# Optimization experiments

Measured on AMD Instinct MI355X. Metric: run time of the kernel, lower is better.

## Reference

```python
import jax, jax.numpy as jnp
import numpy as np

T, I, H, O, M = 1024, 128, 512, 512, 32768
BETA = 8.0


def setup_inputs() -> dict:
    key = jax.random.key(0)
    ks = jax.random.split(key, 8)
    s = 0.05  # small init scale to keep tanh unsaturated
    return {
        "inp": jax.random.normal(ks[0], (T, I), jnp.float32),
        "x_obs": jax.nn.softmax(jax.random.normal(ks[1], (T, O), jnp.float32), axis=-1),
        "patterns": jax.random.normal(ks[2], (M, O + H), jnp.float32),  # stored [x | g] slots
        "last_hidden": jnp.zeros((H,), jnp.float32),
        "W_ih": jax.random.normal(ks[3], (H, I), jnp.float32) * s,
        "W_hh": jax.random.normal(ks[4], (H, H), jnp.float32) * s,
        "b_ih": jax.random.normal(ks[5], (H,), jnp.float32) * s,
        "b_hh": jax.random.normal(ks[6], (H,), jnp.float32) * s,
    }


def _retrieve(query, keys, values, beta):
    # distance-based slot attention: softmax(-beta * ||q - k||^2) @ values
    # sqdist via the expanded form to avoid a [T, M, D] intermediate
    d = (jnp.sum(query * query, axis=-1, keepdims=True)
         + jnp.sum(keys * keys, axis=-1)[None, :]
         - 2.0 * query @ keys.T)  # [T, M]
    w = jax.nn.softmax(-beta * d, axis=-1)
    return w @ values  # [T, O]


def reference(inp, x_obs, patterns, last_hidden, W_ih, W_hh, b_ih, b_hh):
    # single-layer tanh RNN (nn.RNN semantics), unbatched [T, I]
    def step(h, x):
        h_new = jnp.tanh(x @ W_ih.T + b_ih + h @ W_hh.T + b_hh)
        return h_new, h_new

    h_last, g_cur = jax.lax.scan(step, last_hidden, inp)  # g_cur: [T, H]

    x_vals = patterns[:, :O]   # stored x-parts
    g_keys = patterns[:, O:]   # stored g-parts
    prob_g = _retrieve(g_cur, g_keys, x_vals, BETA)   # index_g=True
    prob_x = _retrieve(x_obs, x_vals, x_vals, BETA)   # index_g=False
    # memory.store(hstack([x_obs, g_cur])) is a pure side effect on the buffer
    # and does not affect this step's outputs.
    return prob_g, prob_x, g_cur, h_last[None, :]
```

## Files before the change

### kernel.cpp

```cpp
#include <hip/hip_runtime.h>
#include <math.h>

#define T_STEPS 1024
#define I_DIM   128
#define H_DIM   512
#define O_DIM   512
#define M_PAT   32768
#define SCAN_WGS 8
#define VT_STR  32800

typedef __attribute__((ext_vector_type(8))) short s16x8;
typedef __attribute__((ext_vector_type(4))) float f32x4;

__device__ __forceinline__ void bf_split(float f, unsigned short& hi, unsigned short& lo) {
  unsigned u = __builtin_bit_cast(unsigned, f);
  hi = (unsigned short)(u >> 16);
  float r = f - __builtin_bit_cast(float, u & 0xFFFF0000u);
  lo = (unsigned short)(__builtin_bit_cast(unsigned, r) >> 16);
}
__device__ __forceinline__ unsigned short f2bf(float f) {
  return (unsigned short)(__builtin_bit_cast(unsigned, f) >> 16);
}
__device__ __forceinline__ float bf2f(unsigned short b) {
  return __builtin_bit_cast(float, ((unsigned)b) << 16);
}

__global__ __launch_bounds__(256) void xw_kernel(const float* __restrict__ inp,
    const float* __restrict__ W_ih, const float* __restrict__ b_ih,
    const float* __restrict__ b_hh, float* __restrict__ xw) {
  int t = blockIdx.x;
  __shared__ float4 xs4[I_DIM / 4];
  if (threadIdx.x < I_DIM / 4)
    xs4[threadIdx.x] = ((const float4*)(inp + (size_t)t * I_DIM))[threadIdx.x];
  __syncthreads();
  for (int j = threadIdx.x; j < H_DIM; j += 256) {
    const float4* w4 = (const float4*)(W_ih + (size_t)j * I_DIM);
    float acc = 0.f;
#pragma unroll
    for (int i = 0; i < I_DIM / 4; i++) {
      float4 w = w4[i]; float4 x = xs4[i];
      acc += w.x * x.x + w.y * x.y + w.z * x.z + w.w * x.w;
    }
    xw[(size_t)t * H_DIM + j] = acc + b_ih[j] + b_hh[j];
  }
}

__global__ __launch_bounds__(256, 1) void scan_kernel(
    const float* __restrict__ W_hh, const float* __restrict__ xw,
    const float* __restrict__ h0, float* __restrict__ g_cur,
    float* __restrict__ h_last, unsigned* __restrict__ sync,
    unsigned* __restrict__ henc) {
  unsigned* cnt  = sync + 64;
  unsigned* dec  = sync + 128;
  __shared__ int role_s;
  if (threadIdx.x == 0) {
    unsigned xcd = __builtin_amdgcn_s_getreg(6164) & 7u;
    unsigned my_idx = __hip_atomic_fetch_add(&cnt[xcd], 1u, __ATOMIC_ACQ_REL,
                                             __HIP_MEMORY_SCOPE_AGENT);
    if (blockIdx.x == 0) {
      int chosen = -1;
      while (chosen < 0) {
        for (int x = 0; x < 8; x++)
          if (__hip_atomic_load(&cnt[x], __ATOMIC_ACQUIRE,
                                __HIP_MEMORY_SCOPE_AGENT) >= 8u) { chosen = x; break; }
        if (chosen < 0) __builtin_amdgcn_s_sleep(2);
      }
      __hip_atomic_store(dec, 1u + (unsigned)chosen, __ATOMIC_RELEASE,
                         __HIP_MEMORY_SCOPE_AGENT);
    }
    unsigned d;
    while ((d = __hip_atomic_load(dec, __ATOMIC_ACQUIRE,
                                  __HIP_MEMORY_SCOPE_AGENT)) == 0u)
      __builtin_amdgcn_s_sleep(2);
    role_s = (xcd == d - 1u && my_idx < 8u) ? (int)my_idx : -1;
  }
  __syncthreads();
  const int role = role_s;
  if (role < 0) return;

  const int lane = threadIdx.x & 63;
  const int part = threadIdx.x >> 6;
  const int row  = role * 64 + lane;

  float4 w[32];
  const float4* wsrc = (const float4*)(W_hh + (size_t)row * H_DIM + part * 128);
#pragma unroll
  for (int i = 0; i < 32; i++) w[i] = wsrc[i];
#pragma unroll
  for (int i = 0; i < 32; i++) {
    asm volatile("" : "+v"(w[i].x), "+v"(w[i].y), "+v"(w[i].z), "+v"(w[i].w));
  }

  __shared__ float h_sf[H_DIM];
  __shared__ float red[4][64];

  float xw_next = xw[row];

  for (int t = 0; t < T_STEPS; t++) {
    float xwv = xw_next;
    if (part == 0 && t + 1 < T_STEPS)
      xw_next = xw[(size_t)(t + 1) * H_DIM + row];

    if (t == 0) {
      h_sf[threadIdx.x]       = h0[threadIdx.x];
      h_sf[256 + threadIdx.x] = h0[256 + threadIdx.x];
    } else {
      const unsigned* src = henc + (size_t)(t - 1) * H_DIM;
      unsigned v0, v1;
      do {
        v0 = __hip_atomic_load(src + threadIdx.x, __ATOMIC_RELAXED,
                               __HIP_MEMORY_SCOPE_AGENT);
      } while (__builtin_bit_cast(float, v0) < 1.0f);
      do {
        v1 = __hip_atomic_load(src + 256 + threadIdx.x, __ATOMIC_RELAXED,
                               __HIP_MEMORY_SCOPE_AGENT);
      } while (__builtin_bit_cast(float, v1) < 1.0f);
      h_sf[threadIdx.x]       = __builtin_bit_cast(float, v0) - 2.0f;
      h_sf[256 + threadIdx.x] = __builtin_bit_cast(float, v1) - 2.0f;
    }
    __syncthreads();

    const float4* h4 = (const float4*)h_sf + part * 32;
    float a0 = 0.f, a1 = 0.f, a2 = 0.f, a3 = 0.f;
#pragma unroll
    for (int i = 0; i < 8; i++) {
      float4 x0 = h4[4 * i], x1 = h4[4 * i + 1], x2 = h4[4 * i + 2], x3 = h4[4 * i + 3];
      float4 w0 = w[4 * i], w1 = w[4 * i + 1], w2 = w[4 * i + 2], w3 = w[4 * i + 3];
      a0 += x0.x * w0.x + x0.y * w0.y + x0.z * w0.z + x0.w * w0.w;
      a1 += x1.x * w1.x + x1.y * w1.y + x1.z * w1.z + x1.w * w1.w;
      a2 += x2.x * w2.x + x2.y * w2.y + x2.z * w2.z + x2.w * w2.w;
      a3 += x3.x * w3.x + x3.y * w3.y + x3.z * w3.z + x3.w * w3.w;
    }
    red[part][lane] = (a0 + a1) + (a2 + a3);
    __syncthreads();

    if (part == 0) {
      float pre = red[0][lane] + red[1][lane] + red[2][lane] + red[3][lane] + xwv;
      float e = __expf(2.f * pre);
      float h = 1.f - 2.f / (e + 1.f);
      __hip_atomic_store(henc + (size_t)t * H_DIM + row,
                         __builtin_bit_cast(unsigned, h + 2.0f),
                         __ATOMIC_RELAXED, __HIP_MEMORY_SCOPE_AGENT);
      g_cur[(size_t)t * H_DIM + row] = h;
      if (t == T_STEPS - 1) h_last[row] = h;
    }
  }
}

__global__ __launch_bounds__(256) void norms_kernel(const float* __restrict__ patterns,
    float* __restrict__ bkx, float* __restrict__ bkg) {
  int lane = threadIdx.x & 63;
  int m = blockIdx.x * 4 + (threadIdx.x >> 6);
  const float4* row = (const float4*)(patterns + (size_t)m * (O_DIM + H_DIM));
  float ax = 0.f, ag = 0.f;
#pragma unroll
  for (int jj = 0; jj < 4; jj++) {
    float4 v = row[lane + 64 * jj];
    float s = v.x * v.x + v.y * v.y + v.z * v.z + v.w * v.w;
    if (jj < 2) ax += s; else ag += s;
  }
#pragma unroll
  for (int off = 1; off < 64; off <<= 1) {
    ax += __shfl_xor(ax, off, 64);
    ag += __shfl_xor(ag, off, 64);
  }
  if (lane == 0) { bkx[m] = 8.f * ax; bkg[m] = 8.f * ag; }
}

__global__ __launch_bounds__(256) void vt_kernel(const float* __restrict__ patterns,
                                                 unsigned short* __restrict__ Vt) {
  __shared__ unsigned short tile[64 * 68];
  int kt = blockIdx.x;
  int vt = blockIdx.y;
#pragma unroll
  for (int i = 0; i < 4; i++) {
    int f = threadIdx.x + 256 * i;
    int key = f >> 4, c4 = f & 15;
    float4 v = *(const float4*)(patterns + (size_t)(kt * 64 + key) * 1024 + vt * 64 + c4 * 4);
    unsigned short* dst = &tile[key * 68 + c4 * 4];
    dst[0] = f2bf(v.x); dst[1] = f2bf(v.y); dst[2] = f2bf(v.z); dst[3] = f2bf(v.w);
  }
  __syncthreads();
  int vd = threadIdx.x >> 2, q4 = threadIdx.x & 3;
  unsigned short tmp[16];
#pragma unroll
  for (int k = 0; k < 16; k++) tmp[k] = tile[(q4 * 16 + k) * 68 + vd];
  size_t ob = (size_t)(vt * 64 + vd) * VT_STR + kt * 64 + q4 * 16;
#pragma unroll
  for (int h = 0; h < 2; h++) {
    s16x8 pk;
#pragma unroll
    for (int j = 0; j < 8; j++) pk[j] = (short)tmp[h * 8 + j];
    *(s16x8*)&Vt[ob + h * 8] = pk;
  }
}

template <bool USE_VT>
__global__ __launch_bounds__(512, 2) void flash_kernel(
    const float* __restrict__ Qg, const float* __restrict__ Qx,
    const float* __restrict__ patterns, const float* __restrict__ bkx,
    const float* __restrict__ bkg, const unsigned short* __restrict__ Vt,
    float* __restrict__ pacc, float* __restrict__ pml, int S) {
  const int bid  = blockIdx.x;
  const int sidx = bid >> 6;
  const int ret  = (bid >> 5) & 1;
  const int qt   = bid & 31;
  const int qbase = qt * 32;

  const float* Qp  = ret ? Qx : Qg;
  const float* Kp  = patterns + (ret ? 0 : O_DIM);
  const float* bkk = ret ? bkx : bkg;

  const int chunk = M_PAT / S;
  const int kbeg = sidx * chunk, kend = kbeg + chunk;

  const int lane = threadIdx.x & 63;
  const int wid  = threadIdx.x >> 6;
  const int qg   = wid >> 2;
  const int kw   = wid & 3;
  const int quad = lane >> 4;
  const int l16  = lane & 15;

  __shared__ unsigned short stage_u16[16384];
  __shared__ unsigned short p_lds[32 * 72];
  __shared__ float mrow_s[32], lrow_s[32], alpha_s[32];
  __shared__ int flag_s;

  const int qrow = qbase + qg * 16 + l16;
  s16x8 qhi[16], qlo[16];
#pragma unroll
  for (int kst = 0; kst < 16; kst++) {
    const float4* src = (const float4*)(Qp + (size_t)qrow * 512 + kst * 32 + quad * 8);
    float4 a = src[0], b = src[1];
    float fv[8] = {a.x, a.y, a.z, a.w, b.x, b.y, b.z, b.w};
    s16x8 h, l;
#pragma unroll
    for (int j = 0; j < 8; j++) {
      unsigned short hb, lb; bf_split(fv[j], hb, lb);
      h[j] = (short)hb; l[j] = (short)lb;
    }
    qhi[kst] = h; qlo[kst] = l;
  }

  if (threadIdx.x < 32) { mrow_s[threadIdx.x] = -INFINITY; lrow_s[threadIdx.x] = 0.f; }

  f32x4 o[8];
#pragma unroll
  for (int nb = 0; nb < 8; nb++) o[nb] = (f32x4){0.f, 0.f, 0.f, 0.f};
  float ov[32];
  if (!USE_VT) {
#pragma unroll
    for (int j = 0; j < 32; j++) ov[j] = 0.f;
  }
  const int row2 = threadIdx.x >> 4;
  const int c0   = threadIdx.x & 15;

  for (int k0 = kbeg; k0 < kend; k0 += 64) {
    f32x4 sc = (f32x4){0.f, 0.f, 0.f, 0.f};
#pragma unroll
    for (int dc = 0; dc < 4; dc++) {
      __syncthreads();
      if (dc == 0 && threadIdx.x == 0) flag_s = 0;
#pragma unroll
      for (int i = 0; i < 2; i++) {
        int oid = threadIdx.x + 512 * i;
        int key = oid >> 4, oct = oid & 15;
        const float4* src = (const float4*)(Kp + (size_t)(k0 + key) * 1024 + dc * 128 + oct * 8);
        float4 a = src[0], b = src[1];
        float fv[8] = {a.x, a.y, a.z, a.w, b.x, b.y, b.z, b.w};
        s16x8 hv, lv;
#pragma unroll
        for (int j = 0; j < 8; j++) {
          unsigned short hb, lb; bf_split(fv[j], hb, lb);
          hv[j] = (short)hb; lv[j] = (short)lb;
        }
        int base = (key * 16 + (oct ^ (key & 7))) * 8;
        *(s16x8*)&stage_u16[base] = hv;
        *(s16x8*)&stage_u16[8192 + base] = lv;
      }
      __syncthreads();
#pragma unroll
      for (int ks = 0; ks < 4; ks++) {
        int kst = dc * 4 + ks;
        int key = kw * 16 + l16;
        int oct = ks * 4 + quad;
        int base = (key * 16 + (oct ^ (key & 7))) * 8;
        s16x8 kh = *(const s16x8*)&stage_u16[base];
        s16x8 kl = *(const s16x8*)&stage_u16[8192 + base];
        sc = __builtin_amdgcn_mfma_f32_16x16x32_bf16(qhi[kst], kh, sc, 0, 0, 0);
        sc = __builtin_amdgcn_mfma_f32_16x16x32_bf16(qlo[kst], kh, sc, 0, 0, 0);
        sc = __builtin_amdgcn_mfma_f32_16x16x32_bf16(qhi[kst], kl, sc, 0, 0, 0);
      }
    }
    float bkv = bkk[k0 + kw * 16 + l16];
    __syncthreads();
    float* S_f = (float*)stage_u16;
#pragma unroll
    for (int r = 0; r < 4; r++)
      S_f[(qg * 16 + quad * 4 + r) * 68 + kw * 16 + l16] = 16.f * sc[r] - bkv;
    __syncthreads();

    float s4[4], p4[4];
#pragma unroll
    for (int c = 0; c < 4; c++) s4[c] = S_f[row2 * 68 + c0 + 16 * c];
    float tmax = fmaxf(fmaxf(s4[0], s4[1]), fmaxf(s4[2], s4[3]));
#pragma unroll
    for (int off = 1; off < 16; off <<= 1) tmax = fmaxf(tmax, __shfl_xor(tmax, off, 16));
    float mold = mrow_s[row2];
    float mnew = fmaxf(mold, tmax);
    float tsum = 0.f;
#pragma unroll
    for (int c = 0; c < 4; c++) { p4[c] = __expf(s4[c] - mnew); tsum += p4[c]; }
#pragma unroll
    for (int off = 1; off < 16; off <<= 1) tsum += __shfl_xor(tsum, off, 16);
#pragma unroll
    for (int c = 0; c < 4; c++) p_lds[row2 * 72 + c0 + 16 * c] = f2bf(p4[c]);
    if (c0 == 0) {
      float al = __expf(mold - mnew);
      alpha_s[row2] = al;
      mrow_s[row2] = mnew;
      lrow_s[row2] = lrow_s[row2] * al + tsum;
      if (tmax > mold - 25.f) flag_s = 1;
    }
    __syncthreads();
    const int doPV = flag_s;

    if (doPV) {
      if (USE_VT) {
        float alr[4];
#pragma unroll
        for (int r = 0; r < 4; r++) alr[r] = alpha_s[qg * 16 + quad * 4 + r];
#pragma unroll
        for (int nb = 0; nb < 8; nb++) {
          o[nb][0] *= alr[0]; o[nb][1] *= alr[1]; o[nb][2] *= alr[2]; o[nb][3] *= alr[3];
        }
#pragma unroll
        for (int ks2 = 0; ks2 < 2; ks2++) {
          s16x8 pf = *(const s16x8*)&p_lds[(qg * 16 + l16) * 72 + ks2 * 32 + quad * 8];
#pragma unroll
          for (int nb = 0; nb < 8; nb++) {
            int vd = kw * 128 + nb * 16 + l16;
            s16x8 vf = *(const s16x8*)(Vt + (size_t)vd * VT_STR + (k0 + ks2 * 32 + quad * 8));
            o[nb] = __builtin_amdgcn_mfma_f32_16x16x32_bf16(pf, vf, o[nb], 0, 0, 0);
          }
        }
      } else {
        float al = alpha_s[row2];
#pragma unroll
        for (int j = 0; j < 32; j++) ov[j] *= al;
        for (int key = 0; key < 64; key++) {
          float w = bf2f(p_lds[row2 * 72 + key]);
          const float4* vsrc = (const float4*)(patterns + (size_t)(k0 + key) * 1024 + c0 * 32);
#pragma unroll
          for (int j = 0; j < 8; j++) {
            float4 v = vsrc[j];
            ov[4 * j + 0] += w * v.x; ov[4 * j + 1] += w * v.y;
            ov[4 * j + 2] += w * v.z; ov[4 * j + 3] += w * v.w;
          }
        }
      }
    }
  }

  __syncthreads();
  size_t pbase = ((size_t)(ret * S + sidx) * T_STEPS + qbase);
  if (USE_VT) {
#pragma unroll
    for (int nb = 0; nb < 8; nb++)
#pragma unroll
      for (int r = 0; r < 4; r++)
        pacc[(pbase + qg * 16 + quad * 4 + r) * 512 + kw * 128 + nb * 16 + l16] = o[nb][r];
  } else {
#pragma unroll
    for (int j = 0; j < 32; j++)
      pacc[(pbase + row2) * 512 + c0 * 32 + j] = ov[j];
  }
  if (threadIdx.x < 32) {
    pml[(pbase + threadIdx.x) * 2]     = mrow_s[threadIdx.x];
    pml[(pbase + threadIdx.x) * 2 + 1] = lrow_s[threadIdx.x];
  }
}

__global__ __launch_bounds__(256) void combine_kernel(
    const float* __restrict__ pacc, const float* __restrict__ pml,
    float* __restrict__ out, int S) {
  int b = blockIdx.x;
  int ret = b >> 10, r = b & 1023;
  float M = -INFINITY;
  for (int s = 0; s < S; s++)
    M = fmaxf(M, pml[((size_t)(ret * S + s) * T_STEPS + r) * 2]);
  float L = 0.f;
  for (int s = 0; s < S; s++) {
    size_t mb = ((size_t)(ret * S + s) * T_STEPS + r) * 2;
    L += pml[mb + 1] * __expf(pml[mb] - M);
  }
  float inv = 1.0f / L;
  for (int cc = threadIdx.x; cc < 512; cc += 256) {
    float acc = 0.f;
    for (int s = 0; s < S; s++) {
      size_t mb = ((size_t)(ret * S + s) * T_STEPS + r) * 2;
      float sc = __expf(pml[mb] - M);
      acc += sc * pacc[((size_t)(ret * S + s) * T_STEPS + r) * 512 + cc];
    }
    out[(size_t)ret * (T_STEPS * O_DIM) + (size_t)r * 512 + cc] = acc * inv;
  }
}

extern "C" void kernel_launch(void* const* d_in, const int* in_sizes, int n_in,
                              void* d_out, int out_size, void* d_ws, size_t ws_size,
                              hipStream_t stream) {
  const float* inp      = (const float*)d_in[0];
  const float* x_obs    = (const float*)d_in[1];
  const float* patterns = (const float*)d_in[2];
  const float* h0       = (const float*)d_in[3];
  const float* W_ih     = (const float*)d_in[4];
  const float* W_hh     = (const float*)d_in[5];
  const float* b_ih     = (const float*)d_in[6];
  const float* b_hh     = (const float*)d_in[7];

  float* out    = (float*)d_out;
  float* g_cur  = out + 1048576;
  float* h_last = out + 1572864;

  char* wsb = (char*)d_ws;
  size_t off = 0;
  auto alloc = [&](size_t bytes) -> char* {
    char* p = wsb + off; off += (bytes + 255) & ~(size_t)255; return p;
  };
  unsigned* sync = (unsigned*)alloc(8192);
  unsigned* henc = (unsigned*)alloc((size_t)T_STEPS * H_DIM * 4);
  float* xw  = (float*)alloc((size_t)T_STEPS * H_DIM * 4);
  float* bkx = (float*)alloc((size_t)M_PAT * 4);
  float* bkg = (float*)alloc((size_t)M_PAT * 4);
  size_t base = off;

  const size_t vt_bytes = (size_t)512 * VT_STR * 2;
  auto pml_bytes  = [](int S) { return (size_t)2 * S * T_STEPS * 2 * 4; };
  auto pacc_bytes = [](int S) { return (size_t)2 * S * T_STEPS * 512 * 4; };

  int S = 4; bool use_vt = false;
  if (base + pml_bytes(4) + pacc_bytes(4) + vt_bytes + 1024 <= ws_size) { S = 4; use_vt = true; }
  else if (base + pml_bytes(2) + pacc_bytes(2) + vt_bytes + 1024 <= ws_size) { S = 2; use_vt = true; }
  else if (base + pml_bytes(4) + pacc_bytes(4) + 1024 <= ws_size) { S = 4; use_vt = false; }
  else if (base + pml_bytes(2) + pacc_bytes(2) + 1024 <= ws_size) { S = 2; use_vt = false; }
  else { S = 1; use_vt = false; }

  float* pml  = (float*)alloc(pml_bytes(S));
  float* pacc = (float*)alloc(pacc_bytes(S));
  unsigned short* Vt = use_vt ? (unsigned short*)alloc(vt_bytes) : (unsigned short*)nullptr;

  hipMemsetAsync(sync, 0, 8192, stream);
  hipMemsetAsync(henc, 0, (size_t)T_STEPS * H_DIM * 4, stream);
  xw_kernel<<<T_STEPS, 256, 0, stream>>>(inp, W_ih, b_ih, b_hh, xw);
  scan_kernel<<<128, 256, 0, stream>>>(W_hh, xw, h0, g_cur, h_last, sync, henc);
  norms_kernel<<<M_PAT / 4, 256, 0, stream>>>(patterns, bkx, bkg);
  if (use_vt) {
    vt_kernel<<<dim3(512, 8), 256, 0, stream>>>(patterns, Vt);
    flash_kernel<true><<<S * 64, 512, 0, stream>>>(g_cur, x_obs, patterns, bkx, bkg,
                                                   Vt, pacc, pml, S);
  } else {
    flash_kernel<false><<<S * 64, 512, 0, stream>>>(g_cur, x_obs, patterns, bkx, bkg,
                                                    nullptr, pacc, pml, S);
  }
  combine_kernel<<<2 * T_STEPS, 256, 0, stream>>>(pacc, pml, out, S);
}
```

Before: 2.621 ms.

## Split scan into 32 single-wave workgroups and drop block barriers

Restructures the sequential RNN scan from 8 workgroups of 4 waves to 32 single-wave workgroups on one XCD. Each wave handles 16 rows, with 4 lanes per row each holding a 128-column slice of W_hh in registers, and reduces with intra-wave shuffles instead of an LDS reduction and __syncthreads. Each lane polls 8 h values at once and writes them to a padded LDS buffer, so the per-step block barriers are replaced by an lgkmcnt wait. The aim is shorter per-step critical-path latency, at the cost of more workgroups polling global memory and more scattered polling loads per lane.

New measurement: 2.624 ms. No clear change (+0.1%).

```diff
diff --git a/kernel.cpp b/kernel.cpp
--- a/kernel.cpp
+++ b/kernel.cpp
@@ -6,7 +6,7 @@
 #define H_DIM   512
 #define O_DIM   512
 #define M_PAT   32768
-#define SCAN_WGS 8
+#define SCAN_ROLES 32
 #define VT_STR  32800
 
 typedef __attribute__((ext_vector_type(8))) short s16x8;
@@ -45,7 +45,7 @@
   }
 }
 
-__global__ __launch_bounds__(256, 1) void scan_kernel(
+__global__ __launch_bounds__(64, 1) void scan_kernel(
     const float* __restrict__ W_hh, const float* __restrict__ xw,
     const float* __restrict__ h0, float* __restrict__ g_cur,
     float* __restrict__ h_last, unsigned* __restrict__ sync,
@@ -62,7 +62,9 @@
       while (chosen < 0) {
         for (int x = 0; x < 8; x++)
           if (__hip_atomic_load(&cnt[x], __ATOMIC_ACQUIRE,
-                                __HIP_MEMORY_SCOPE_AGENT) >= 8u) { chosen = x; break; }
+                                __HIP_MEMORY_SCOPE_AGENT) >= (unsigned)SCAN_ROLES) {
+            chosen = x; break;
+          }
         if (chosen < 0) __builtin_amdgcn_s_sleep(2);
       }
       __hip_atomic_store(dec, 1u + (unsigned)chosen, __ATOMIC_RELEASE,
@@ -72,18 +74,18 @@
     while ((d = __hip_atomic_load(dec, __ATOMIC_ACQUIRE,
                                   __HIP_MEMORY_SCOPE_AGENT)) == 0u)
       __builtin_amdgcn_s_sleep(2);
-    role_s = (xcd == d - 1u && my_idx < 8u) ? (int)my_idx : -1;
+    role_s = (xcd == d - 1u && my_idx < (unsigned)SCAN_ROLES) ? (int)my_idx : -1;
   }
   __syncthreads();
   const int role = role_s;
   if (role < 0) return;
 
-  const int lane = threadIdx.x & 63;
-  const int part = threadIdx.x >> 6;
-  const int row  = role * 64 + lane;
+  const int lane = threadIdx.x;
+  const int g    = lane & 3;
+  const int row  = role * 16 + (lane >> 2);
 
   float4 w[32];
-  const float4* wsrc = (const float4*)(W_hh + (size_t)row * H_DIM + part * 128);
+  const float4* wsrc = (const float4*)(W_hh + (size_t)row * H_DIM + g * 128);
 #pragma unroll
   for (int i = 0; i < 32; i++) w[i] = wsrc[i];
 #pragma unroll
@@ -91,51 +93,64 @@
     asm volatile("" : "+v"(w[i].x), "+v"(w[i].y), "+v"(w[i].z), "+v"(w[i].w));
   }
 
-  __shared__ float h_sf[H_DIM];
-  __shared__ float red[4][64];
+  __shared__ float hbuf[528];
 
   float xw_next = xw[row];
 
   for (int t = 0; t < T_STEPS; t++) {
     float xwv = xw_next;
-    if (part == 0 && t + 1 < T_STEPS)
+    if (t + 1 < T_STEPS)
       xw_next = xw[(size_t)(t + 1) * H_DIM + row];
 
     if (t == 0) {
-      h_sf[threadIdx.x]       = h0[threadIdx.x];
-      h_sf[256 + threadIdx.x] = h0[256 + threadIdx.x];
+#pragma unroll
+      for (int j = 0; j < 8; j++) {
+        int c = 64 * j + lane;
+        hbuf[c + 4 * (j >> 1)] = h0[c];
+      }
     } else {
       const unsigned* src = henc + (size_t)(t - 1) * H_DIM;
-      unsigned v0, v1;
-      do {
-        v0 = __hip_atomic_load(src + threadIdx.x, __ATOMIC_RELAXED,
-                               __HIP_MEMORY_SCOPE_AGENT);
-      } while (__builtin_bit_cast(float, v0) < 1.0f);
-      do {
-        v1 = __hip_atomic_load(src + 256 + threadIdx.x, __ATOMIC_RELAXED,
-                               __HIP_MEMORY_SCOPE_AGENT);
-      } while (__builtin_bit_cast(float, v1) < 1.0f);
-      h_sf[threadIdx.x]       = __builtin_bit_cast(float, v0) - 2.0f;
-      h_sf[256 + threadIdx.x] = __builtin_bit_cast(float, v1) - 2.0f;
-    }
-    __syncthreads();
-
-    const float4* h4 = (const float4*)h_sf + part * 32;
+      unsigned u[8];
+#pragma unroll
+      for (int j = 0; j < 8; j++)
+        u[j] = __hip_atomic_load(src + 64 * j + lane, __ATOMIC_RELAXED,
+                                 __HIP_MEMORY_SCOPE_AGENT);
+      bool again = true;
+      while (again) {
+        again = false;
+#pragma unroll
+        for (int j = 0; j < 8; j++)
+          if (__builtin_bit_cast(float, u[j]) < 1.0f) {
+            again = true;
+            u[j] = __hip_atomic_load(src + 64 * j + lane, __ATOMIC_RELAXED,
+                                     __HIP_MEMORY_SCOPE_AGENT);
+          }
+      }
+#pragma unroll
+      for (int j = 0; j < 8; j++) {
+        int c = 64 * j + lane;
+        hbuf[c + 4 * (j >> 1)] = __builtin_bit_cast(float, u[j]) - 2.0f;
+      }
+    }
+    asm volatile("s_waitcnt lgkmcnt(0)" ::: "memory");
+
+    const float4* hb = (const float4*)&hbuf[g * 132];
     float a0 = 0.f, a1 = 0.f, a2 = 0.f, a3 = 0.f;
 #pragma unroll
     for (int i = 0; i < 8; i++) {
-      float4 x0 = h4[4 * i], x1 = h4[4 * i + 1], x2 = h4[4 * i + 2], x3 = h4[4 * i + 3];
+      float4 x0 = hb[4 * i], x1 = hb[4 * i + 1], x2 = hb[4 * i + 2], x3 = hb[4 * i + 3];
       float4 w0 = w[4 * i], w1 = w[4 * i + 1], w2 = w[4 * i + 2], w3 = w[4 * i + 3];
       a0 += x0.x * w0.x + x0.y * w0.y + x0.z * w0.z + x0.w * w0.w;
       a1 += x1.x * w1.x + x1.y * w1.y + x1.z * w1.z + x1.w * w1.w;
       a2 += x2.x * w2.x + x2.y * w2.y + x2.z * w2.z + x2.w * w2.w;
       a3 += x3.x * w3.x + x3.y * w3.y + x3.z * w3.z + x3.w * w3.w;
     }
-    red[part][lane] = (a0 + a1) + (a2 + a3);
-    __syncthreads();
-
-    if (part == 0) {
-      float pre = red[0][lane] + red[1][lane] + red[2][lane] + red[3][lane] + xwv;
+    float a = (a0 + a1) + (a2 + a3);
+    a += __shfl_xor(a, 1, 4);
+    a += __shfl_xor(a, 2, 4);
+
+    if (g == 0) {
+      float pre = a + xwv;
       float e = __expf(2.f * pre);
       float h = 1.f - 2.f / (e + 1.f);
       __hip_atomic_store(henc + (size_t)t * H_DIM + row,
@@ -452,7 +467,7 @@
   hipMemsetAsync(sync, 0, 8192, stream);
   hipMemsetAsync(henc, 0, (size_t)T_STEPS * H_DIM * 4, stream);
   xw_kernel<<<T_STEPS, 256, 0, stream>>>(inp, W_ih, b_ih, b_hh, xw);
-  scan_kernel<<<128, 256, 0, stream>>>(W_hh, xw, h0, g_cur, h_last, sync, henc);
+  scan_kernel<<<1024, 64, 0, stream>>>(W_hh, xw, h0, g_cur, h_last, sync, henc);
   norms_kernel<<<M_PAT / 4, 256, 0, stream>>>(patterns, bkx, bkg);
   if (use_vt) {
     vt_kernel<<<dim3(512, 8), 256, 0, stream>>>(patterns, Vt);
```
